# Optimization experiments

Measured on AMD Instinct MI355X. Metric: run time of the kernel, lower is better.

The kernel has to match this reference:

```python
import jax, jax.numpy as jnp
import numpy as np
from jax.scipy.special import logsumexp

N, K, D = 131072, 256, 32


def setup_inputs() -> dict:
    key = jax.random.key(0)
    k1, k2, k3 = jax.random.split(key, 3)
    points = jax.random.normal(k1, (N, D), dtype=jnp.float32)
    centers = jax.random.uniform(k2, (K, D), dtype=jnp.float32)
    # well-conditioned inverse-sqrt covariances (original used 15*I; scaled to
    # avoid float32 overflow in sqrt(det(covs_inv)) for D=32)
    covs_inv_sqrt = (0.5 * jnp.broadcast_to(jnp.eye(D, dtype=jnp.float32), (K, D, D))
                     + 0.02 * jax.random.normal(k3, (K, D, D), dtype=jnp.float32))
    weights = jnp.ones((K,), dtype=jnp.float32)
    threshold = jnp.zeros((1,), dtype=jnp.float32)
    return {"points": points, "centers": centers,
            "covs_inv_sqrt": covs_inv_sqrt, "weights": weights,
            "threshold": threshold}


def reference(points, centers, covs_inv_sqrt, weights, threshold):
    # refresh(): equal_clusters=True branch
    w = jnp.abs(weights)
    center_prs = w / (w.sum() + 1e-30)                       # [K]
    covs_inv = jnp.einsum('kde,kfe->kdf', covs_inv_sqrt, covs_inv_sqrt)  # [K,D,D]
    coefs = center_prs * jnp.sqrt(jnp.linalg.det(covs_inv))  # [K]

    # pairwise weighted sqdist: q_ij = (x_i - c_j)^T A_j (x_i - c_j)
    B = covs_inv.reshape(K, D * D)                           # [K, D*D]
    X2 = (points[:, :, None] * points[:, None, :]).reshape(N, D * D)  # [N, D*D]
    t_xAx = X2 @ B.T                                         # [N, K]
    m = jnp.einsum('kde,ke->kd', covs_inv, centers)          # A_j c_j, [K,D]
    t_xAc = points @ m.T                                     # [N, K]
    t_cAc = jnp.einsum('kd,kd->k', m, centers)               # [K]
    d_ij = -0.5 * (t_xAx - 2.0 * t_xAc + t_cAc[None, :])     # [N, K]

    # weighted logsumexp over centers, then subtract threshold
    ll = logsumexp(d_ij, axis=1, b=coefs[None, :])           # [N]
    return ll[:, None] - threshold[0]                        # [N, 1]
```

## Files before the change

kernel.cpp:

```cpp
#include <hip/hip_runtime.h>
#include <math.h>

#define NPTS 131072
#define KCOMP 256
#define DIM 32
#define NREAL 560
#define NCH 18
#define PSIF_BYTES 294912
#define WS_NEED (PSIF_BYTES + KCOMP * 4)

typedef __attribute__((ext_vector_type(8))) short short8;
typedef __attribute__((ext_vector_type(16))) float f32x16;

__device__ __forceinline__ unsigned short f2bf(float v) {
    unsigned u = __float_as_uint(v);
    u += 0x7fffu + ((u >> 16) & 1u);
    return (unsigned short)(u >> 16);
}

__device__ __forceinline__ unsigned pkbf(float lo, float hi) {
#if __has_builtin(__builtin_amdgcn_perm)
    const unsigned a = __float_as_uint(hi) + 0x8000u;
    const unsigned b = __float_as_uint(lo) + 0x8000u;
    return __builtin_amdgcn_perm(a, b, 0x07060302u);
#else
    return (unsigned)f2bf(lo) | ((unsigned)f2bf(hi) << 16);
#endif
}

__device__ __forceinline__ void barrier_lds() {
    asm volatile("s_waitcnt lgkmcnt(0)\ns_barrier" ::: "memory");
}

constexpr int PfxT(int d) { return 32 * d - (d * (d - 1)) / 2; }
constexpr int rowT(int p) { int d = 0; while (d < 31 && PfxT(d + 1) <= p) ++d; return d; }
constexpr int colT(int p) { return rowT(p) + (p - PfxT(rowT(p))); }

template<int P, int J>
__device__ __forceinline__ float genOne(const float (&x)[DIM]) {
    constexpr int p = P + J;
    if constexpr (p >= NREAL) {
        return 0.f;
    } else if constexpr (p >= 528) {
        return x[p - 528];
    } else {
        constexpr int d = rowT(p);
        constexpr int f = colT(p);
        static_assert(d >= 0 && d < 32 && f >= d && f < 32, "bad feature map");
        return x[d] * x[f];
    }
}

__global__ __launch_bounds__(256) void gmm_pre(
    const float* __restrict__ S,
    const float* __restrict__ centers,
    const float* __restrict__ weights,
    unsigned short* __restrict__ PsiF,
    float* __restrict__ kc2)
{
    __shared__ float Sl[DIM][DIM + 1];
    __shared__ float As[DIM][DIM + 1];
    __shared__ float cl[DIM], ml[DIM];
    __shared__ float red[256];

    const int k = blockIdx.x, tid = threadIdx.x;

    for (int idx = tid; idx < DIM * DIM; idx += 256)
        Sl[idx >> 5][idx & 31] = S[(size_t)k * DIM * DIM + idx];
    if (tid < DIM) cl[tid] = centers[k * DIM + tid];
    __syncthreads();

    for (int idx = tid; idx < DIM * DIM; idx += 256) {
        const int d = idx >> 5, f = idx & 31;
        float a = 0.f;
#pragma unroll
        for (int e = 0; e < DIM; ++e) a = fmaf(Sl[d][e], Sl[f][e], a);
        As[d][f] = a;
    }
    __syncthreads();

    if (tid < DIM) {
        float mv = 0.f;
#pragma unroll
        for (int f = 0; f < DIM; ++f) mv = fmaf(As[tid][f], cl[f], mv);
        ml[tid] = mv;
    }
    __syncthreads();

    for (int p = tid; p < NREAL; p += 256) {
        float val;
        if (p < 528) {
            int d = 0, pr = 0;
            while (pr + (32 - d) <= p) { pr += (32 - d); ++d; }
            const int f = d + (p - pr);
            val = (f == d) ? -0.5f * As[d][d] : -As[d][f];
        } else {
            val = ml[p - 528];
        }
        const int c = p >> 6, kk = p & 63;
        const int s = kk >> 4, qq = (kk >> 3) & 1, j = kk & 7;
        const int ct = k >> 5, ll = qq * 32 + (k & 31);
        const int g = c * 2048 + (s * 8 + ct) * 64 + ll;
        PsiF[(size_t)g * 8 + j] = f2bf(val);
    }

    red[tid] = fabsf(weights[tid]);
    __syncthreads();
    for (int off = 128; off > 0; off >>= 1) {
        if (tid < off) red[tid] += red[tid + off];
        __syncthreads();
    }
    const float wsum = red[0];

    for (int j = 0; j < DIM - 1; ++j) {
        const float inv = 1.0f / As[j][j];
        for (int idx = tid; idx < DIM * DIM; idx += 256) {
            const int r = idx >> 5, c = idx & 31;
            if (r > j && c > j)
                As[r][c] = fmaf(-As[r][j] * inv, As[j][c], As[r][c]);
        }
        __syncthreads();
    }

    if (tid < DIM) red[tid] = __logf(As[tid][tid]);
    __syncthreads();
    if (tid == 0) {
        float sl = 0.f;
        for (int j = 0; j < DIM; ++j) sl += red[j];
        float cac = 0.f;
        for (int d2 = 0; d2 < DIM; ++d2) cac = fmaf(ml[d2], cl[d2], cac);
        kc2[k] = __logf(fabsf(weights[k])) - __logf(wsum + 1e-30f)
               + 0.5f * sl - 0.5f * cac;
    }
}

template<int P>
__device__ __forceinline__ void genQuad(const float (&x)[DIM], float* v) {
    v[0] = genOne<P, 0>(x);
    v[1] = genOne<P, 1>(x);
    v[2] = genOne<P, 2>(x);
    v[3] = genOne<P, 3>(x);
}

template<int CH, int SS>
__device__ __forceinline__ void genSiteW(const float (&x)[DIM], uint4* sA4, int l) {
    float v[8];
    genQuad<CH * 32 + SS * 8>(x, v);
    genQuad<CH * 32 + SS * 8 + 4>(x, v + 4);
    uint4 u;
    u.x = pkbf(v[0], v[1]);
    u.y = pkbf(v[2], v[3]);
    u.z = pkbf(v[4], v[5]);
    u.w = pkbf(v[6], v[7]);
    uint4* base = sA4 + (CH & 1) * 256;
    base[(((SS >> 1) * 2 + (l >> 5)) << 6) + (SS & 1) * 32 + (l & 31)] = u;
}

template<int CH>
__device__ __forceinline__ void genChunkW(const float (&x)[DIM], uint4* sA4,
                                          int w, int l) {
    if constexpr (CH < 17) {
        if      (w == 0) genSiteW<CH, 0>(x, sA4, l);
        else if (w == 1) genSiteW<CH, 1>(x, sA4, l);
        else if (w == 2) genSiteW<CH, 2>(x, sA4, l);
        else             genSiteW<CH, 3>(x, sA4, l);
    } else {
        if      (w == 0) genSiteW<CH, 0>(x, sA4, l);
        else if (w == 1) genSiteW<CH, 1>(x, sA4, l);
    }
}

template<int C>
__device__ __forceinline__ void readA(const uint4* sA4, uint4 (&ar)[4], int l) {
    const uint4* aa = sA4 + (C & 1) * 256;
    ar[0] = aa[0 * 64 + l];
    ar[1] = aa[1 * 64 + l];
    if constexpr (C < 17) {
        ar[2] = aa[2 * 64 + l];
        ar[3] = aa[3 * 64 + l];
    }
}

template<int C>
__device__ __forceinline__ void loadB(const uint4* __restrict__ PsiF4,
                                      uint4 (&st)[4], int l, int cgp) {
    const uint4* p = PsiF4 + C * 1024 + (cgp * 2) * 64 + l;
    st[0] = p[0];
    st[1] = p[64];
    if constexpr (C < 17) {
        st[2] = p[512];
        st[3] = p[512 + 64];
    }
}

template<int C>
__device__ __forceinline__ void doChunk(const float (&x)[DIM],
    uint4* sA4, const uint4* __restrict__ PsiF4,
    uint4 (&aReg)[4], uint4 (&cur)[4], uint4 (&nxt)[4],
    f32x16 (&acc)[2][2], int l, int w)
{

    if constexpr (C + 1 < NCH) loadB<C + 1>(PsiF4, nxt, l, w);

    if constexpr (C + 1 < NCH) genChunkW<C + 1>(x, sA4, w, l);

    constexpr int NS = (C < 17) ? 2 : 1;
#pragma unroll
    for (int s2 = 0; s2 < NS; ++s2) {
        short8 f0 = __builtin_bit_cast(short8, aReg[s2 * 2 + 0]);
        short8 f1 = __builtin_bit_cast(short8, aReg[s2 * 2 + 1]);
#pragma unroll
        for (int cj = 0; cj < 2; ++cj) {
            short8 psi = __builtin_bit_cast(short8, cur[s2 * 2 + cj]);
            acc[0][cj] = __builtin_amdgcn_mfma_f32_32x32x16_bf16(psi, f0, acc[0][cj], 0, 0, 0);
            acc[1][cj] = __builtin_amdgcn_mfma_f32_32x32x16_bf16(psi, f1, acc[1][cj], 0, 0, 0);
        }
    }

    if constexpr (C + 1 < NCH) {
        barrier_lds();
        readA<C + 1>(sA4, aReg, l);
    }
}

__global__ __launch_bounds__(256, 3) void gmm_mfma(
    const float* __restrict__ points,
    const unsigned short* __restrict__ PsiF,
    const float* __restrict__ kc2,
    const float* __restrict__ thr,
    float* __restrict__ out)
{
    __shared__ uint4 sA4[512];
    __shared__ float sM[64][4];
    __shared__ float sS[64][4];

    const int t = threadIdx.x;
    const int w = t >> 6, l = t & 63;

    const uint4* PsiF4 = (const uint4*)PsiF;

    float x[DIM];
    const float4* px = (const float4*)(points + ((size_t)blockIdx.x * 64 + l) * DIM);
#pragma unroll
    for (int j2 = 0; j2 < 8; ++j2) {
        float4 v = px[j2];
        x[4 * j2 + 0] = v.x; x[4 * j2 + 1] = v.y;
        x[4 * j2 + 2] = v.z; x[4 * j2 + 3] = v.w;
    }

    f32x16 acc[2][2];
#pragma unroll
    for (int ri = 0; ri < 2; ++ri)
#pragma unroll
        for (int cj = 0; cj < 2; ++cj)
#pragma unroll
            for (int r = 0; r < 16; ++r) acc[ri][cj][r] = 0.f;

    uint4 stA[4], stB[4], aReg[4];
    loadB<0>(PsiF4, stA, l, w);

    genChunkW<0>(x, sA4, w, l);
    barrier_lds();
    readA<0>(sA4, aReg, l);

    doChunk<0>(x, sA4, PsiF4, aReg, stA, stB, acc, l, w);
    doChunk<1>(x, sA4, PsiF4, aReg, stB, stA, acc, l, w);
    doChunk<2>(x, sA4, PsiF4, aReg, stA, stB, acc, l, w);
    doChunk<3>(x, sA4, PsiF4, aReg, stB, stA, acc, l, w);
    doChunk<4>(x, sA4, PsiF4, aReg, stA, stB, acc, l, w);
    doChunk<5>(x, sA4, PsiF4, aReg, stB, stA, acc, l, w);
    doChunk<6>(x, sA4, PsiF4, aReg, stA, stB, acc, l, w);
    doChunk<7>(x, sA4, PsiF4, aReg, stB, stA, acc, l, w);
    doChunk<8>(x, sA4, PsiF4, aReg, stA, stB, acc, l, w);
    doChunk<9>(x, sA4, PsiF4, aReg, stB, stA, acc, l, w);
    doChunk<10>(x, sA4, PsiF4, aReg, stA, stB, acc, l, w);
    doChunk<11>(x, sA4, PsiF4, aReg, stB, stA, acc, l, w);
    doChunk<12>(x, sA4, PsiF4, aReg, stA, stB, acc, l, w);
    doChunk<13>(x, sA4, PsiF4, aReg, stB, stA, acc, l, w);
    doChunk<14>(x, sA4, PsiF4, aReg, stA, stB, acc, l, w);
    doChunk<15>(x, sA4, PsiF4, aReg, stB, stA, acc, l, w);
    doChunk<16>(x, sA4, PsiF4, aReg, stA, stB, acc, l, w);
    doChunk<17>(x, sA4, PsiF4, aReg, stB, stA, acc, l, w);

    const int hi = l >> 5;
    float mr[2] = { -INFINITY, -INFINITY };
#pragma unroll
    for (int cj = 0; cj < 2; ++cj) {
        const float* kp = kc2 + (w * 2 + cj) * 32 + 4 * hi;
        const float4 q0 = *(const float4*)(kp);
        const float4 q1 = *(const float4*)(kp + 8);
        const float4 q2 = *(const float4*)(kp + 16);
        const float4 q3 = *(const float4*)(kp + 24);
#pragma unroll
        for (int ri = 0; ri < 2; ++ri) {
#define KADD(R, QC) { float _v = acc[ri][cj][R] + (QC); acc[ri][cj][R] = _v; mr[ri] = fmaxf(mr[ri], _v); }
            KADD(0, q0.x)  KADD(1, q0.y)  KADD(2, q0.z)  KADD(3, q0.w)
            KADD(4, q1.x)  KADD(5, q1.y)  KADD(6, q1.z)  KADD(7, q1.w)
            KADD(8, q2.x)  KADD(9, q2.y)  KADD(10, q2.z) KADD(11, q2.w)
            KADD(12, q3.x) KADD(13, q3.y) KADD(14, q3.z) KADD(15, q3.w)
#undef KADD
        }
    }
#pragma unroll
    for (int ri = 0; ri < 2; ++ri) {
        float m = fmaxf(mr[ri], __shfl_xor(mr[ri], 32, 64));
        float sv = 0.f;
#pragma unroll
        for (int cj = 0; cj < 2; ++cj)
#pragma unroll
            for (int rg = 0; rg < 16; ++rg)
                sv += __expf(acc[ri][cj][rg] - m);
        sv += __shfl_xor(sv, 32, 64);
        if (l < 32) {
            sM[ri * 32 + l][w] = m;
            sS[ri * 32 + l][w] = sv;
        }
    }
    __syncthreads();

    if (t < 64) {
        const float m0 = sM[t][0], m1 = sM[t][1], m2 = sM[t][2], m3 = sM[t][3];
        const float M = fmaxf(fmaxf(m0, m1), fmaxf(m2, m3));
        const float Sv = sS[t][0] * __expf(m0 - M) + sS[t][1] * __expf(m1 - M)
                       + sS[t][2] * __expf(m2 - M) + sS[t][3] * __expf(m3 - M);
        out[(size_t)blockIdx.x * 64 + t] = M + __logf(Sv) - thr[0];
    }
}

extern "C" void kernel_launch(void* const* d_in, const int* in_sizes, int n_in,
                              void* d_out, int out_size, void* d_ws, size_t ws_size,
                              hipStream_t stream) {
    const float* points  = (const float*)d_in[0];
    const float* centers = (const float*)d_in[1];
    const float* covs    = (const float*)d_in[2];
    const float* weights = (const float*)d_in[3];
    const float* thr     = (const float*)d_in[4];
    float* out = (float*)d_out;

    unsigned short* PsiF = (unsigned short*)d_ws;
    float* kc2 = (float*)((char*)d_ws + PSIF_BYTES);

    gmm_pre<<<KCOMP, 256, 0, stream>>>(covs, centers, weights, PsiF, kc2);
    gmm_mfma<<<NPTS / 64, 256, 0, stream>>>(points, PsiF, kc2, thr, out);
}
```

Before: 129.5 us.

## Process two chunks per barrier with quad-buffered LDS feature tiles

Restructures the main loop so each period generates and consumes two feature chunks, cutting LDS barriers from one per chunk to one per pair. The shared feature buffer grows from two to four slots, and an extra register set holds the second chunk's A fragments. The goal is to reduce barrier stalls and let more generation overlap MFMA work. The cost is more LDS and VGPR use, which may hurt occupancy at the launch bound of 3 blocks.

```diff
diff --git a/kernel.cpp b/kernel.cpp
--- a/kernel.cpp
+++ b/kernel.cpp
@@ -152,7 +152,7 @@
     u.y = pkbf(v[2], v[3]);
     u.z = pkbf(v[4], v[5]);
     u.w = pkbf(v[6], v[7]);
-    uint4* base = sA4 + (CH & 1) * 256;
+    uint4* base = sA4 + ((CH >> 1) & 1) * 512 + (CH & 1) * 256;
     base[(((SS >> 1) * 2 + (l >> 5)) << 6) + (SS & 1) * 32 + (l & 31)] = u;
 }
 
@@ -172,7 +172,7 @@
 
 template<int C>
 __device__ __forceinline__ void readA(const uint4* sA4, uint4 (&ar)[4], int l) {
-    const uint4* aa = sA4 + (C & 1) * 256;
+    const uint4* aa = sA4 + ((C >> 1) & 1) * 512 + (C & 1) * 256;
     ar[0] = aa[0 * 64 + l];
     ar[1] = aa[1 * 64 + l];
     if constexpr (C < 17) {
@@ -194,32 +194,42 @@
 }
 
 template<int C>
-__device__ __forceinline__ void doChunk(const float (&x)[DIM],
+__device__ __forceinline__ void mfmaChunk(const uint4 (&aR)[4], const uint4 (&bR)[4],
+                                          f32x16 (&acc)[2][2]) {
+    constexpr int NS = (C < 17) ? 2 : 1;
+#pragma unroll
+    for (int s2 = 0; s2 < NS; ++s2) {
+        short8 f0 = __builtin_bit_cast(short8, aR[s2 * 2 + 0]);
+        short8 f1 = __builtin_bit_cast(short8, aR[s2 * 2 + 1]);
+#pragma unroll
+        for (int cj = 0; cj < 2; ++cj) {
+            short8 psi = __builtin_bit_cast(short8, bR[s2 * 2 + cj]);
+            acc[0][cj] = __builtin_amdgcn_mfma_f32_32x32x16_bf16(psi, f0, acc[0][cj], 0, 0, 0);
+            acc[1][cj] = __builtin_amdgcn_mfma_f32_32x32x16_bf16(psi, f1, acc[1][cj], 0, 0, 0);
+        }
+    }
+}
+
+template<int P>
+__device__ __forceinline__ void doPeriod(const float (&x)[DIM],
     uint4* sA4, const uint4* __restrict__ PsiF4,
-    uint4 (&aReg)[4], uint4 (&cur)[4], uint4 (&nxt)[4],
+    uint4 (&aA)[4], uint4 (&aB)[4], uint4 (&bA)[4], uint4 (&bB)[4],
     f32x16 (&acc)[2][2], int l, int w)
 {
-
-    if constexpr (C + 1 < NCH) loadB<C + 1>(PsiF4, nxt, l, w);
-
-    if constexpr (C + 1 < NCH) genChunkW<C + 1>(x, sA4, w, l);
-
-    constexpr int NS = (C < 17) ? 2 : 1;
-#pragma unroll
-    for (int s2 = 0; s2 < NS; ++s2) {
-        short8 f0 = __builtin_bit_cast(short8, aReg[s2 * 2 + 0]);
-        short8 f1 = __builtin_bit_cast(short8, aReg[s2 * 2 + 1]);
-#pragma unroll
-        for (int cj = 0; cj < 2; ++cj) {
-            short8 psi = __builtin_bit_cast(short8, cur[s2 * 2 + cj]);
-            acc[0][cj] = __builtin_amdgcn_mfma_f32_32x32x16_bf16(psi, f0, acc[0][cj], 0, 0, 0);
-            acc[1][cj] = __builtin_amdgcn_mfma_f32_32x32x16_bf16(psi, f1, acc[1][cj], 0, 0, 0);
-        }
-    }
-
-    if constexpr (C + 1 < NCH) {
+    constexpr int c0 = 2 * P, c1 = 2 * P + 1;
+
+    loadB<c1>(PsiF4, bB, l, w);
+    if constexpr (c0 + 2 < NCH) genChunkW<c0 + 2>(x, sA4, w, l);
+    mfmaChunk<c0>(aA, bA, acc);
+
+    if constexpr (c1 + 1 < NCH) loadB<c1 + 1>(PsiF4, bA, l, w);
+    if constexpr (c0 + 3 < NCH) genChunkW<c0 + 3>(x, sA4, w, l);
+    mfmaChunk<c1>(aB, bB, acc);
+
+    if constexpr (c1 + 1 < NCH) {
         barrier_lds();
-        readA<C + 1>(sA4, aReg, l);
+        readA<c0 + 2>(sA4, aA, l);
+        readA<c0 + 3>(sA4, aB, l);
     }
 }
 
@@ -230,7 +240,7 @@
     const float* __restrict__ thr,
     float* __restrict__ out)
 {
-    __shared__ uint4 sA4[512];
+    __shared__ uint4 sA4[1024];
     __shared__ float sM[64][4];
     __shared__ float sS[64][4];
 
@@ -256,31 +266,24 @@
 #pragma unroll
             for (int r = 0; r < 16; ++r) acc[ri][cj][r] = 0.f;
 
-    uint4 stA[4], stB[4], aReg[4];
-    loadB<0>(PsiF4, stA, l, w);
+    uint4 aA[4], aB[4], bA[4], bB[4];
+    loadB<0>(PsiF4, bA, l, w);
 
     genChunkW<0>(x, sA4, w, l);
+    genChunkW<1>(x, sA4, w, l);
     barrier_lds();
-    readA<0>(sA4, aReg, l);
-
-    doChunk<0>(x, sA4, PsiF4, aReg, stA, stB, acc, l, w);
-    doChunk<1>(x, sA4, PsiF4, aReg, stB, stA, acc, l, w);
-    doChunk<2>(x, sA4, PsiF4, aReg, stA, stB, acc, l, w);
-    doChunk<3>(x, sA4, PsiF4, aReg, stB, stA, acc, l, w);
-    doChunk<4>(x, sA4, PsiF4, aReg, stA, stB, acc, l, w);
-    doChunk<5>(x, sA4, PsiF4, aReg, stB, stA, acc, l, w);
-    doChunk<6>(x, sA4, PsiF4, aReg, stA, stB, acc, l, w);
-    doChunk<7>(x, sA4, PsiF4, aReg, stB, stA, acc, l, w);
-    doChunk<8>(x, sA4, PsiF4, aReg, stA, stB, acc, l, w);
-    doChunk<9>(x, sA4, PsiF4, aReg, stB, stA, acc, l, w);
-    doChunk<10>(x, sA4, PsiF4, aReg, stA, stB, acc, l, w);
-    doChunk<11>(x, sA4, PsiF4, aReg, stB, stA, acc, l, w);
-    doChunk<12>(x, sA4, PsiF4, aReg, stA, stB, acc, l, w);
-    doChunk<13>(x, sA4, PsiF4, aReg, stB, stA, acc, l, w);
-    doChunk<14>(x, sA4, PsiF4, aReg, stA, stB, acc, l, w);
-    doChunk<15>(x, sA4, PsiF4, aReg, stB, stA, acc, l, w);
-    doChunk<16>(x, sA4, PsiF4, aReg, stA, stB, acc, l, w);
-    doChunk<17>(x, sA4, PsiF4, aReg, stB, stA, acc, l, w);
+    readA<0>(sA4, aA, l);
+    readA<1>(sA4, aB, l);
+
+    doPeriod<0>(x, sA4, PsiF4, aA, aB, bA, bB, acc, l, w);
+    doPeriod<1>(x, sA4, PsiF4, aA, aB, bA, bB, acc, l, w);
+    doPeriod<2>(x, sA4, PsiF4, aA, aB, bA, bB, acc, l, w);
+    doPeriod<3>(x, sA4, PsiF4, aA, aB, bA, bB, acc, l, w);
+    doPeriod<4>(x, sA4, PsiF4, aA, aB, bA, bB, acc, l, w);
+    doPeriod<5>(x, sA4, PsiF4, aA, aB, bA, bB, acc, l, w);
+    doPeriod<6>(x, sA4, PsiF4, aA, aB, bA, bB, acc, l, w);
+    doPeriod<7>(x, sA4, PsiF4, aA, aB, bA, bB, acc, l, w);
+    doPeriod<8>(x, sA4, PsiF4, aA, aB, bA, bB, acc, l, w);
 
     const int hi = l >> 5;
     float mr[2] = { -INFINITY, -INFINITY };
```

New measurement: 135.2 us. +4.4%, slower.
